# Kernel optimization log

Hardware: AMD Instinct MI355X
Metric: run time of the kernel (lower is better)

## Reference

```python
import jax, jax.numpy as jnp
import numpy as np

# Physics constants (forward defaults of My_loss.forward)
RHO_L_ATM = 851.6
BETA_L_ATM = 1466.96
AIR_FRACTION = 0.005
RHO_G_ATM = 1.225
POLYTROPIC_INDEX = 1.0
P_ATM = 0.101325
P_MIN = 1.0
PHYSICS_WEIGHT = 0.5
CLS_WEIGHT = 0.5
PT_EPS = 1e-12

B, S = 512, 16384


def setup_inputs() -> dict:
    key = jax.random.key(0)
    k = jax.random.split(key, 6)
    return {
        "p_pred": jax.random.normal(k[0], (B, S, 1), jnp.float32),
        "p_t_pred": jax.random.normal(k[1], (B, S, 1), jnp.float32),
        "fault_logit": jax.random.normal(k[2], (B, 1), jnp.float32),
        "targets_fault": jax.random.uniform(k[3], (B,), jnp.float32),
        "mdot_A": jax.random.normal(k[4], (B, S), jnp.float32),
        "targets_p_orig": jax.random.normal(k[5], (B, S, 1), jnp.float32),
        "V": jnp.ones((1,), jnp.float32),
    }


def _drho_mix_dp(p):
    # mixture_density_derivative with bulk_modulus_model='const',
    # air_dissolution_model='off', air_fraction != 0 (default 0.005).
    # -> theta = 1, dtheta_dp = 0.
    p_used = jnp.maximum(p, P_MIN)
    r = AIR_FRACTION / (1.0 - AIR_FRACTION)
    p_denom = r * (P_ATM / p_used) ** (1.0 / POLYTROPIC_INDEX)  # theta = 1
    p_ratio = p_denom / (p_used * POLYTROPIC_INDEX)
    exp_term = jnp.exp(-(p_used - P_ATM) / BETA_L_ATM) / BETA_L_ATM
    rho_mix_init = RHO_L_ATM + RHO_G_ATM * r
    denominator = BETA_L_ATM * exp_term + p_denom
    return rho_mix_init * (exp_term + p_ratio) / denominator ** 2


def reference(p_pred, p_t_pred, fault_logit, targets_fault, mdot_A, targets_p_orig, V):
    b, s = p_pred.shape[0], p_pred.shape[1]
    pp = p_pred[..., 0]          # [B,S]
    pt = p_t_pred[..., 0]        # [B,S]
    tgt = targets_p_orig[..., 0] # [B,S]

    mask = jnp.abs(pt) >= PT_EPS  # elements with tiny derivative are skipped

    drho = _drho_mix_dp(pp * 0.1)
    physics_res = V[0] * drho * pt - mdot_A
    loss_physics = jnp.sum(jnp.where(mask, jnp.abs(physics_res), 0.0)) / (b * s)
    loss_M = jnp.sum(jnp.where(mask, jnp.abs(tgt - pp), 0.0)) / (b * s)

    # BCEWithLogitsLoss (mean reduction), numerically stable
    x = fault_logit[:, 0]
    y = targets_fault
    loss_cls = jnp.mean(jnp.maximum(x, 0.0) - x * y + jnp.log1p(jnp.exp(-jnp.abs(x))))

    total = loss_M + PHYSICS_WEIGHT * loss_physics + CLS_WEIGHT * loss_cls
    return jnp.stack([total, loss_M, loss_physics, loss_cls])
```

## Files before the change

kernel.cpp:

```cpp
#include <hip/hip_runtime.h>
#include <math.h>

#define THREADS 256
#define BLOCKS  2048
#define STRIDE  (BLOCKS * THREADS)
#define FTHREADS 1024

__device__ __forceinline__ float wave_reduce(float v) {
    #pragma unroll
    for (int off = 32; off > 0; off >>= 1)
        v += __shfl_down(v, off, 64);
    return v;
}

__device__ __forceinline__ void accum_elem(float pp, float pt, float md, float tg,
                                           float V, float& phys, float& lm) {
    constexpr float P_ATM    = 0.101325f;
    constexpr float BETA     = 1466.96f;
    constexpr float INV_BETA = 1.0f / 1466.96f;
    constexpr float R_FRAC   = 0.005f / 0.995f;
    constexpr float C_RP     = R_FRAC * P_ATM;
    constexpr float RHO_MIX  = 851.6f + 1.225f * R_FRAC;
    constexpr float PT_EPS   = 1e-12f;

    float p_used  = fmaxf(pp * 0.1f, 1.0f);
    float inv_pu  = __builtin_amdgcn_rcpf(p_used);
    float p_denom = C_RP * inv_pu;
    float p_ratio = p_denom * inv_pu;
    float e       = __expf((P_ATM - p_used) * INV_BETA) * INV_BETA;
    float denom   = BETA * e + p_denom;
    float inv_d   = __builtin_amdgcn_rcpf(denom);
    float drho    = RHO_MIX * (e + p_ratio) * inv_d * inv_d;

    float res  = V * drho * pt - md;
    bool  m    = fabsf(pt) >= PT_EPS;
    phys += m ? fabsf(res)     : 0.0f;
    lm   += m ? fabsf(tg - pp) : 0.0f;
}

__device__ __forceinline__ void accum_vec4(const float4& a, const float4& b,
                                           const float4& c, const float4& d,
                                           float V, float& phys, float& lm) {
    accum_elem(a.x, b.x, c.x, d.x, V, phys, lm);
    accum_elem(a.y, b.y, c.y, d.y, V, phys, lm);
    accum_elem(a.z, b.z, c.z, d.z, V, phys, lm);
    accum_elem(a.w, b.w, c.w, d.w, V, phys, lm);
}

__global__ __launch_bounds__(THREADS, 8) void loss_main_kernel(
    const float4* __restrict__ pp4,
    const float4* __restrict__ pt4,
    const float4* __restrict__ md4,
    const float4* __restrict__ tg4,
    const float*  __restrict__ Vp,
    float2*       __restrict__ partials,
    int n4)
{
    const float V = Vp[0];
    float phys = 0.0f;
    float lm   = 0.0f;

    const int tid = blockIdx.x * THREADS + threadIdx.x;

    if (tid + STRIDE < n4) {
        float4 a0 = pp4[tid];
        float4 b0 = pt4[tid];
        float4 c0 = md4[tid];
        float4 d0 = tg4[tid];
        float4 a1 = pp4[tid + STRIDE];
        float4 b1 = pt4[tid + STRIDE];
        float4 c1 = md4[tid + STRIDE];
        float4 d1 = tg4[tid + STRIDE];

        for (int i = tid + 2 * STRIDE; i < n4; i += STRIDE) {
            float4 a2 = pp4[i];
            float4 b2 = pt4[i];
            float4 c2 = md4[i];
            float4 d2 = tg4[i];
            accum_vec4(a0, b0, c0, d0, V, phys, lm);
            a0 = a1; b0 = b1; c0 = c1; d0 = d1;
            a1 = a2; b1 = b2; c1 = c2; d1 = d2;
        }
        accum_vec4(a0, b0, c0, d0, V, phys, lm);
        accum_vec4(a1, b1, c1, d1, V, phys, lm);
    } else if (tid < n4) {
        float4 a = pp4[tid];
        float4 b = pt4[tid];
        float4 c = md4[tid];
        float4 d = tg4[tid];
        accum_vec4(a, b, c, d, V, phys, lm);
    }

    phys = wave_reduce(phys);
    lm   = wave_reduce(lm);

    __shared__ float sp[4];
    __shared__ float sl[4];
    int lane = threadIdx.x & 63;
    int w    = threadIdx.x >> 6;
    if (lane == 0) { sp[w] = phys; sl[w] = lm; }
    __syncthreads();
    if (threadIdx.x == 0) {
        float P = sp[0] + sp[1] + sp[2] + sp[3];
        float L = sl[0] + sl[1] + sl[2] + sl[3];
        partials[blockIdx.x] = make_float2(P, L);
    }
}

__global__ __launch_bounds__(FTHREADS) void loss_finish_kernel(
    const float4* __restrict__ partials4, int nblk4,
    const float*  __restrict__ logit,
    const float*  __restrict__ yf,
    int nb,
    float*        __restrict__ out,
    float inv_ns)
{
    float phys = 0.0f, lm = 0.0f, cls = 0.0f;

    for (int i = threadIdx.x; i < nblk4; i += FTHREADS) {
        float4 p = partials4[i];
        phys += p.x + p.z;
        lm   += p.y + p.w;
    }
    for (int i = threadIdx.x; i < nb; i += FTHREADS) {
        float x = logit[i];
        float y = yf[i];
        cls += fmaxf(x, 0.0f) - x * y + log1pf(__expf(-fabsf(x)));
    }

    phys = wave_reduce(phys);
    lm   = wave_reduce(lm);
    cls  = wave_reduce(cls);

    __shared__ float sp[16], sl[16], sc[16];
    int lane = threadIdx.x & 63;
    int w    = threadIdx.x >> 6;
    if (lane == 0) { sp[w] = phys; sl[w] = lm; sc[w] = cls; }
    __syncthreads();
    if (threadIdx.x == 0) {
        float P = 0.0f, L = 0.0f, C = 0.0f;
        #pragma unroll
        for (int k = 0; k < 16; ++k) { P += sp[k]; L += sl[k]; C += sc[k]; }

        float loss_physics = P * inv_ns;
        float loss_M       = L * inv_ns;
        float loss_cls     = C / (float)nb;

        out[0] = loss_M + 0.5f * loss_physics + 0.5f * loss_cls;
        out[1] = loss_M;
        out[2] = loss_physics;
        out[3] = loss_cls;
    }
}

extern "C" void kernel_launch(void* const* d_in, const int* in_sizes, int n_in,
                              void* d_out, int out_size, void* d_ws, size_t ws_size,
                              hipStream_t stream) {
    const float* p_pred   = (const float*)d_in[0];
    const float* p_t_pred = (const float*)d_in[1];
    const float* logit    = (const float*)d_in[2];
    const float* yfault   = (const float*)d_in[3];
    const float* mdot_A   = (const float*)d_in[4];
    const float* tgt_p    = (const float*)d_in[5];
    const float* V        = (const float*)d_in[6];

    int n  = in_sizes[0];
    int nb = in_sizes[3];
    int n4 = n / 4;

    float2* partials = (float2*)d_ws;

    loss_main_kernel<<<BLOCKS, THREADS, 0, stream>>>(
        (const float4*)p_pred, (const float4*)p_t_pred,
        (const float4*)mdot_A, (const float4*)tgt_p,
        V, partials, n4);

    loss_finish_kernel<<<1, FTHREADS, 0, stream>>>(
        (const float4*)partials, BLOCKS / 2, logit, yfault, nb,
        (float*)d_out, 1.0f / (float)n);
}
```

Baseline: 32.48 us.

## Replace grid-stride prefetch loop with one float4 per thread grid

Removes the fixed-size persistent grid with a two-deep software-prefetch pipeline and launches one thread per float4, sizing the grid from the problem. This relies on hardware occupancy rather than explicit prefetch to hide memory latency and removes the loop overhead. It produces many more block partials (8192), which the finish kernel must reduce and the workspace must hold.

```diff
diff --git a/kernel.cpp b/kernel.cpp
--- a/kernel.cpp
+++ b/kernel.cpp
@@ -2,8 +2,6 @@
 #include <math.h>
 
 #define THREADS 256
-#define BLOCKS  2048
-#define STRIDE  (BLOCKS * THREADS)
 #define FTHREADS 1024
 
 __device__ __forceinline__ float wave_reduce(float v) {
@@ -38,16 +36,7 @@
     lm   += m ? fabsf(tg - pp) : 0.0f;
 }
 
-__device__ __forceinline__ void accum_vec4(const float4& a, const float4& b,
-                                           const float4& c, const float4& d,
-                                           float V, float& phys, float& lm) {
-    accum_elem(a.x, b.x, c.x, d.x, V, phys, lm);
-    accum_elem(a.y, b.y, c.y, d.y, V, phys, lm);
-    accum_elem(a.z, b.z, c.z, d.z, V, phys, lm);
-    accum_elem(a.w, b.w, c.w, d.w, V, phys, lm);
-}
-
-__global__ __launch_bounds__(THREADS, 8) void loss_main_kernel(
+__global__ __launch_bounds__(THREADS) void loss_main_kernel(
     const float4* __restrict__ pp4,
     const float4* __restrict__ pt4,
     const float4* __restrict__ md4,
@@ -60,35 +49,17 @@
     float phys = 0.0f;
     float lm   = 0.0f;
 
-    const int tid = blockIdx.x * THREADS + threadIdx.x;
+    const int i = blockIdx.x * THREADS + threadIdx.x;
 
-    if (tid + STRIDE < n4) {
-        float4 a0 = pp4[tid];
-        float4 b0 = pt4[tid];
-        float4 c0 = md4[tid];
-        float4 d0 = tg4[tid];
-        float4 a1 = pp4[tid + STRIDE];
-        float4 b1 = pt4[tid + STRIDE];
-        float4 c1 = md4[tid + STRIDE];
-        float4 d1 = tg4[tid + STRIDE];
-
-        for (int i = tid + 2 * STRIDE; i < n4; i += STRIDE) {
-            float4 a2 = pp4[i];
-            float4 b2 = pt4[i];
-            float4 c2 = md4[i];
-            float4 d2 = tg4[i];
-            accum_vec4(a0, b0, c0, d0, V, phys, lm);
-            a0 = a1; b0 = b1; c0 = c1; d0 = d1;
-            a1 = a2; b1 = b2; c1 = c2; d1 = d2;
-        }
-        accum_vec4(a0, b0, c0, d0, V, phys, lm);
-        accum_vec4(a1, b1, c1, d1, V, phys, lm);
-    } else if (tid < n4) {
-        float4 a = pp4[tid];
-        float4 b = pt4[tid];
-        float4 c = md4[tid];
-        float4 d = tg4[tid];
-        accum_vec4(a, b, c, d, V, phys, lm);
+    if (i < n4) {
+        float4 a = pp4[i];
+        float4 b = pt4[i];
+        float4 c = md4[i];
+        float4 d = tg4[i];
+        accum_elem(a.x, b.x, c.x, d.x, V, phys, lm);
+        accum_elem(a.y, b.y, c.y, d.y, V, phys, lm);
+        accum_elem(a.z, b.z, c.z, d.z, V, phys, lm);
+        accum_elem(a.w, b.w, c.w, d.w, V, phys, lm);
     }
 
     phys = wave_reduce(phys);
@@ -168,14 +139,16 @@
     int nb = in_sizes[3];
     int n4 = n / 4;
 
+    int blocks = (n4 + THREADS - 1) / THREADS;
+
     float2* partials = (float2*)d_ws;
 
-    loss_main_kernel<<<BLOCKS, THREADS, 0, stream>>>(
+    loss_main_kernel<<<blocks, THREADS, 0, stream>>>(
         (const float4*)p_pred, (const float4*)p_t_pred,
         (const float4*)mdot_A, (const float4*)tgt_p,
         V, partials, n4);
 
     loss_finish_kernel<<<1, FTHREADS, 0, stream>>>(
-        (const float4*)partials, BLOCKS / 2, logit, yfault, nb,
+        (const float4*)partials, blocks / 2, logit, yfault, nb,
         (float*)d_out, 1.0f / (float)n);
 }
```

New measurement: 28.50 us. 12.3% less time.
